# Optimization experiments

Measured on AMD Instinct MI355X. Metric: run time of the kernel, lower is better.

Reference implementation:

```python
import jax, jax.numpy as jnp
import numpy as np

B, T, D, H = 2, 2048, 1024, 16
HD = D // H


def setup_inputs() -> dict:
    key = jax.random.key(0)
    ks = jax.random.split(key, 8)
    s = 1.0 / np.sqrt(D)
    x = jax.random.normal(ks[0], (B, T, D), dtype=jnp.float32)
    # causal additive mask, as in Whisper: -inf-like on strict upper triangle
    mask = jnp.triu(jnp.full((T, T), -1e9, dtype=jnp.float32), k=1)
    Wq = jax.random.normal(ks[1], (D, D), dtype=jnp.float32) * s
    bq = jax.random.normal(ks[2], (D,), dtype=jnp.float32) * 0.02
    Wk = jax.random.normal(ks[3], (D, D), dtype=jnp.float32) * s  # key has no bias
    Wv = jax.random.normal(ks[4], (D, D), dtype=jnp.float32) * s
    bv = jax.random.normal(ks[5], (D,), dtype=jnp.float32) * 0.02
    Wo = jax.random.normal(ks[6], (D, D), dtype=jnp.float32) * s
    bo = jax.random.normal(ks[7], (D,), dtype=jnp.float32) * 0.02
    return {"x": x, "mask": mask, "Wq": Wq, "bq": bq, "Wk": Wk,
            "Wv": Wv, "bv": bv, "Wo": Wo, "bo": bo}


def reference(x, mask, Wq, bq, Wk, Wv, bv, Wo, bo):
    # Linear layers (torch F.linear: x @ W.T + b)
    q = x @ Wq.T + bq                      # [B, T, D]
    k = x @ Wk.T                           # [B, T, D] (no bias)
    v = x @ Wv.T + bv                      # [B, T, D]

    scale = (D // H) ** (-0.25)
    qh = q.reshape(B, T, H, HD) * scale    # [B, T, H, hd]
    kh = k.reshape(B, T, H, HD) * scale
    vh = v.reshape(B, T, H, HD)

    qk = jnp.einsum("bqhd,bkhd->bhqk", qh, kh)        # [B, H, T, T]
    qk = qk + mask[:T, :T]
    w = jax.nn.softmax(qk.astype(jnp.float32), axis=-1).astype(q.dtype)
    wv = jnp.einsum("bhqk,bkhd->bqhd", w, vh).reshape(B, T, D)
    return wv @ Wo.T + bo
```

## Files before the change

kernel.cpp:

```cpp
#include <hip/hip_runtime.h>
#include <hip/hip_bf16.h>

#define B_ 2
#define T_ 2048
#define D_ 1024
#define H_ 16
#define HD_ 64

typedef __attribute__((ext_vector_type(8))) short bf16x8;
typedef __attribute__((ext_vector_type(4))) short bf16x4;
typedef __attribute__((ext_vector_type(4))) float f32x4;
typedef __attribute__((ext_vector_type(4))) unsigned int u32x4;

__device__ __forceinline__ short f2bf(float f) {
  unsigned int u = __builtin_bit_cast(unsigned int, f);
  u += 0x7fffu + ((u >> 16) & 1u);
  return (short)(u >> 16);
}

__device__ __forceinline__ unsigned cvtpk(float lo, float hi) {
  unsigned r;
  asm("v_cvt_pk_bf16_f32 %0, %1, %2" : "=v"(r) : "v"(lo), "v"(hi));
  return r;
}

__device__ __forceinline__ float ex2(float x) {
  float r;
  asm("v_exp_f32 %0, %1" : "=v"(r) : "v"(x));
  return r;
}

__device__ __forceinline__ void gl16(const short* g, short* l) {
  __builtin_amdgcn_global_load_lds(
      (const __attribute__((address_space(1))) void*)g,
      (__attribute__((address_space(3))) void*)l, 16, 0, 0);
}

__global__ void cast_all(const float* __restrict__ x,
                         const float* __restrict__ w0, const float* __restrict__ w1,
                         const float* __restrict__ w2, const float* __restrict__ w3,
                         short* __restrict__ out) {
  int i = (blockIdx.x * blockDim.x + threadIdx.x) * 8;
  const float* src;
  int off;
  if (i < 4194304) { src = x; off = i; }
  else {
    int j = i - 4194304;
    int seg = j >> 20;
    src = (seg == 0) ? w0 : (seg == 1) ? w1 : (seg == 2) ? w2 : w3;
    off = j & 1048575;
  }
  float4 a = *(const float4*)(src + off);
  float4 b = *(const float4*)(src + off + 4);
  bf16x8 o;
  o[0] = f2bf(a.x); o[1] = f2bf(a.y); o[2] = f2bf(a.z); o[3] = f2bf(a.w);
  o[4] = f2bf(b.x); o[5] = f2bf(b.y); o[6] = f2bf(b.z); o[7] = f2bf(b.w);
  *(bf16x8*)(out + i) = o;
}

__launch_bounds__(256, 4)
__global__ void gemm_qkv(const short* __restrict__ A, const short* __restrict__ W,
                         const float* __restrict__ bq, const float* __restrict__ bv,
                         short* __restrict__ Qb, short* __restrict__ Kb,
                         short* __restrict__ Vtb) {
  __shared__ short As[2][128 * 32];
  __shared__ short Bs[2][128 * 32];
  const int xcd = blockIdx.x & 7, g = blockIdx.x >> 3;
  const int bm = (xcd >> 1) * 8 + (g & 7);
  const int bn = (xcd & 1) * 12 + (g >> 3);
  const int tid = threadIdx.x, lane = tid & 63, w = tid >> 6;
  const int wr = w >> 1, wc = w & 1;
  const int lrow = lane & 15, lhi = lane >> 4;
  const int srow = lane >> 2, sch = lane & 3;
  const int swz = (lrow >> 1) & 3;

  f32x4 acc[4][4] = {};
  auto STAGE = [&](int kt, int buf) {
#pragma unroll
    for (int i = 0; i < 2; ++i) {
      int row = w * 32 + i * 16 + srow;
      int csrc = (sch ^ ((row >> 1) & 3)) * 8;
      gl16(A + (size_t)(bm * 128 + row) * 1024 + kt + csrc,
           &As[buf][(w * 32 + i * 16) * 32]);
      gl16(W + (size_t)(bn * 128 + row) * 1024 + kt + csrc,
           &Bs[buf][(w * 32 + i * 16) * 32]);
    }
  };

  STAGE(0, 0);
  for (int t = 0; t < 32; ++t) {
    const int buf = t & 1;
    if (t < 31) {
      STAGE((t + 1) * 32, buf ^ 1);
      asm volatile("s_waitcnt vmcnt(4)" ::: "memory");
    } else {
      asm volatile("s_waitcnt vmcnt(0)" ::: "memory");
    }
    __builtin_amdgcn_s_barrier();
    bf16x8 af[4], bfr[4];
#pragma unroll
    for (int i = 0; i < 4; ++i) {
      af[i]  = *(const bf16x8*)(&As[buf][(wr * 64 + i * 16 + lrow) * 32 + ((lhi ^ swz) * 8)]);
      bfr[i] = *(const bf16x8*)(&Bs[buf][(wc * 64 + i * 16 + lrow) * 32 + ((lhi ^ swz) * 8)]);
    }
#pragma unroll
    for (int i = 0; i < 4; ++i)
#pragma unroll
      for (int j = 0; j < 4; ++j)
        acc[i][j] = __builtin_amdgcn_mfma_f32_16x16x32_bf16(af[i], bfr[j],
                                                            acc[i][j], 0, 0, 0);
    asm volatile("s_waitcnt lgkmcnt(0)" ::: "memory");
    __builtin_amdgcn_s_barrier();
  }

#pragma unroll
  for (int i = 0; i < 4; ++i)
#pragma unroll
    for (int j = 0; j < 4; ++j) {
      const int m0 = bm * 128 + wr * 64 + i * 16 + lhi * 4;
      const int n = bn * 128 + wc * 64 + j * 16 + lrow;
      const int seg = n >> 10, nloc = n & 1023;
      const int h = nloc >> 6, hd = nloc & 63;
      const int b = m0 >> 11, t0 = m0 & 2047;
      if (seg == 0) {
        float bb = bq[nloc];
#pragma unroll
        for (int r = 0; r < 4; ++r)
          Qb[((size_t)(b * H_ + h) * T_ + t0 + r) * HD_ + hd] =
              f2bf((acc[i][j][r] + bb) * 0.180336880f);
      } else if (seg == 1) {
#pragma unroll
        for (int r = 0; r < 4; ++r)
          Kb[((size_t)(b * H_ + h) * T_ + t0 + r) * HD_ + hd] = f2bf(acc[i][j][r]);
      } else {
        float bb = bv[nloc];
        bf16x4 ov;
#pragma unroll
        for (int r = 0; r < 4; ++r) ov[r] = f2bf(acc[i][j][r] + bb);
        const int c = (i >> 1) * 32 + lhi * 8 + (i & 1) * 4;
        *(bf16x4*)(Vtb + ((size_t)(b * H_ + h) * HD_ + hd) * T_ + (t0 & ~63) + c) = ov;
      }
    }
}

__launch_bounds__(256, 3)
__global__ void gemm_o(const short* __restrict__ A, const short* __restrict__ W,
                       const float* __restrict__ bias, float* __restrict__ out) {
  __shared__ short As[2][64 * 64];
  __shared__ short Bs[2][128 * 64];
  const int xcd = blockIdx.x & 7, g = blockIdx.x >> 3;
  const int bm = (xcd >> 1) * 16 + (g & 15);
  const int bn = (xcd & 1) * 4 + (g >> 4);
  const int tid = threadIdx.x, lane = tid & 63, w = tid >> 6;
  const int wr = w >> 1, wc = w & 1;
  const int lrow = lane & 15, lhi = lane >> 4;
  const int srow = lane >> 3, sch = lane & 7;
  const int swz = (lrow & 7) << 3;

  f32x4 acc[2][4] = {};
  auto STAGE = [&](int kt, int buf) {
#pragma unroll
    for (int i = 0; i < 2; ++i) {
      int row = w * 16 + i * 8 + srow;
      gl16(A + (size_t)(bm * 64 + row) * 1024 + kt + ((sch ^ (row & 7)) * 8),
           &As[buf][(w * 16 + i * 8) * 64]);
    }
#pragma unroll
    for (int i = 0; i < 4; ++i) {
      int row = w * 32 + i * 8 + srow;
      gl16(W + (size_t)(bn * 128 + row) * 1024 + kt + ((sch ^ (row & 7)) * 8),
           &Bs[buf][(w * 32 + i * 8) * 64]);
    }
  };

  STAGE(0, 0);
  for (int t = 0; t < 16; ++t) {
    const int buf = t & 1;
    if (t < 15) {
      STAGE((t + 1) * 64, buf ^ 1);
      asm volatile("s_waitcnt vmcnt(6)" ::: "memory");
    } else {
      asm volatile("s_waitcnt vmcnt(0)" ::: "memory");
    }
    __builtin_amdgcn_s_barrier();
    bf16x8 af[2][2], bfr[2][4];
#pragma unroll
    for (int ks = 0; ks < 2; ++ks) {
#pragma unroll
      for (int i = 0; i < 2; ++i)
        af[ks][i] = *(const bf16x8*)(&As[buf][(wr * 32 + i * 16 + lrow) * 64 + ((ks * 32 + lhi * 8) ^ swz)]);
#pragma unroll
      for (int j = 0; j < 4; ++j)
        bfr[ks][j] = *(const bf16x8*)(&Bs[buf][(wc * 64 + j * 16 + lrow) * 64 + ((ks * 32 + lhi * 8) ^ swz)]);
    }
#pragma unroll
    for (int ks = 0; ks < 2; ++ks)
#pragma unroll
      for (int i = 0; i < 2; ++i)
#pragma unroll
        for (int j = 0; j < 4; ++j)
          acc[i][j] = __builtin_amdgcn_mfma_f32_16x16x32_bf16(af[ks][i], bfr[ks][j],
                                                              acc[i][j], 0, 0, 0);
    asm volatile("s_waitcnt lgkmcnt(0)" ::: "memory");
    __builtin_amdgcn_s_barrier();
  }

#pragma unroll
  for (int i = 0; i < 2; ++i)
#pragma unroll
    for (int j = 0; j < 4; ++j) {
      const int m0 = bm * 64 + wr * 32 + i * 16 + lhi * 4;
      const int n = bn * 128 + wc * 64 + j * 16 + lrow;
      const float bb = bias[n];
#pragma unroll
      for (int r = 0; r < 4; ++r)
        out[(size_t)(m0 + r) * 1024 + n] = acc[i][j][r] + bb;
    }
}

__launch_bounds__(256, 4)
__global__ void attn_kernel(const short* __restrict__ Q, const short* __restrict__ K,
                            const short* __restrict__ Vt, short* __restrict__ Ob) {
  __shared__ short Ks_[2][64 * 64];
  __shared__ short Vs_[2][64 * 64];
  const int tid = threadIdx.x, lane = tid & 63, w = tid >> 6;
  const int lrow = lane & 15, lhi = lane >> 4;
  const int bid = blockIdx.x;
  const int bh = (bid & 7) * 4 + ((bid >> 3) & 3);
  const int x = bid >> 5, g = x & 7, q = x >> 3;
  const int tile = ((q & 1) ? (7 - g) : g) * 4 + q;
  const int b = bh >> 4, h = bh & 15;
  const short* Kbh = K + (size_t)bh * T_ * HD_;
  const short* Vbh = Vt + (size_t)bh * HD_ * T_;

  bf16x8 qf[2];
#pragma unroll
  for (int ks = 0; ks < 2; ++ks)
    qf[ks] = *(const bf16x8*)(Q + ((size_t)bh * T_ + tile * 64 + w * 16 + lrow) * HD_ + ks * 32 + lhi * 8);

  f32x4 oacc[4] = {};
  float lrun = 0.f;
  const int qlocal = w * 16 + lrow;
  const int srow8 = lane >> 3, sch = lane & 7;
  const int swz = (lrow & 7) << 3;

  auto STAGE = [&](int kb, int buf) {
#pragma unroll
    for (int pass = 0; pass < 2; ++pass) {
      int row = pass * 32 + w * 8 + srow8;
      int csrc = (sch ^ (row & 7)) * 8;
      gl16(Kbh + (size_t)(kb * 64 + row) * HD_ + csrc, &Ks_[buf][(pass * 32 + w * 8) * 64]);
      gl16(Vbh + (size_t)row * T_ + kb * 64 + csrc, &Vs_[buf][(pass * 32 + w * 8) * 64]);
    }
  };

  STAGE(0, 0);
  int cur = 0;
  for (int kb = 0; kb <= tile; ++kb) {
    asm volatile("s_waitcnt vmcnt(0) lgkmcnt(0)" ::: "memory");
    __builtin_amdgcn_s_barrier();
    asm volatile("" ::: "memory");
    const short* Kc = Ks_[cur];
    const short* Vc = Vs_[cur];
    bf16x8 kf[4][2];
#pragma unroll
    for (int n = 0; n < 4; ++n)
#pragma unroll
      for (int ks = 0; ks < 2; ++ks)
        kf[n][ks] = *(const bf16x8*)(Kc + (n * 16 + lrow) * 64 + ((ks * 32 + lhi * 8) ^ swz));
    bf16x8 vf[4][2];
#pragma unroll
    for (int j = 0; j < 4; ++j)
#pragma unroll
      for (int ks = 0; ks < 2; ++ks)
        vf[j][ks] = *(const bf16x8*)(Vc + (j * 16 + lrow) * 64 + ((ks * 32 + lhi * 8) ^ swz));
    if (kb < tile) STAGE(kb + 1, cur ^ 1);

    f32x4 s[4] = {};
    __builtin_amdgcn_s_setprio(1);
#pragma unroll
    for (int n = 0; n < 4; ++n)
#pragma unroll
      for (int ks = 0; ks < 2; ++ks)
        s[n] = __builtin_amdgcn_mfma_f32_16x16x32_bf16(kf[n][ks], qf[ks], s[n], 0, 0, 0);
    __builtin_amdgcn_s_setprio(0);

    if (kb == tile) {
#pragma unroll
      for (int n = 0; n < 4; ++n)
#pragma unroll
        for (int r = 0; r < 4; ++r)
          if (n * 16 + lhi * 4 + r > qlocal) s[n][r] = -1e9f;
    }

    float p[4][4];
    float ls = 0.f;
#pragma unroll
    for (int n = 0; n < 4; ++n)
#pragma unroll
      for (int r = 0; r < 4; ++r) {
        float e = ex2(s[n][r]);
        p[n][r] = e;
        ls += e;
      }
    lrun += ls;

    u32x4 pw0, pw1;
    pw0[0] = cvtpk(p[0][0], p[0][1]); pw0[1] = cvtpk(p[0][2], p[0][3]);
    pw0[2] = cvtpk(p[1][0], p[1][1]); pw0[3] = cvtpk(p[1][2], p[1][3]);
    pw1[0] = cvtpk(p[2][0], p[2][1]); pw1[1] = cvtpk(p[2][2], p[2][3]);
    pw1[2] = cvtpk(p[3][0], p[3][1]); pw1[3] = cvtpk(p[3][2], p[3][3]);
    bf16x8 pf0 = __builtin_bit_cast(bf16x8, pw0);
    bf16x8 pf1 = __builtin_bit_cast(bf16x8, pw1);

    __builtin_amdgcn_s_setprio(1);
#pragma unroll
    for (int j = 0; j < 4; ++j) {
      oacc[j] = __builtin_amdgcn_mfma_f32_16x16x32_bf16(vf[j][0], pf0, oacc[j], 0, 0, 0);
      oacc[j] = __builtin_amdgcn_mfma_f32_16x16x32_bf16(vf[j][1], pf1, oacc[j], 0, 0, 0);
    }
    __builtin_amdgcn_s_setprio(0);
    cur ^= 1;
  }

  lrun += __shfl_xor(lrun, 16);
  lrun += __shfl_xor(lrun, 32);
  float inv = 1.0f / lrun;
  const int t = tile * 64 + qlocal;
#pragma unroll
  for (int j = 0; j < 4; ++j) {
    bf16x4 ok;
#pragma unroll
    for (int r = 0; r < 4; ++r) ok[r] = f2bf(oacc[j][r] * inv);
    *(bf16x4*)(Ob + (size_t)(b * T_ + t) * D_ + h * 64 + j * 16 + lhi * 4) = ok;
  }
}

extern "C" void kernel_launch(void* const* d_in, const int* in_sizes, int n_in,
                              void* d_out, int out_size, void* d_ws, size_t ws_size,
                              hipStream_t stream) {
  const float* x  = (const float*)d_in[0];
  const float* Wq = (const float*)d_in[2];
  const float* bq = (const float*)d_in[3];
  const float* Wk = (const float*)d_in[4];
  const float* Wv = (const float*)d_in[5];
  const float* bv = (const float*)d_in[6];
  const float* Wo = (const float*)d_in[7];
  const float* bo = (const float*)d_in[8];
  float* out = (float*)d_out;

  const int MT = B_ * T_;
  short* xb  = (short*)d_ws;
  short* wqb = xb  + (size_t)MT * D_;
  short* wob = wqb + (size_t)3 * D_ * D_;
  short* Qb  = wob + (size_t)D_ * D_;
  short* Kb  = Qb  + (size_t)MT * D_;
  short* Vtb = Kb  + (size_t)MT * D_;
  short* Ab  = Vtb + (size_t)MT * D_;

  cast_all<<<(8 * 1048576) / (256 * 8), 256, 0, stream>>>(x, Wq, Wk, Wv, Wo, xb);

  gemm_qkv<<<(MT / 128) * 24, 256, 0, stream>>>(xb, wqb, bq, bv, Qb, Kb, Vtb);

  attn_kernel<<<B_ * H_ * 32, 256, 0, stream>>>(Qb, Kb, Vtb, Ab);

  gemm_o<<<(MT / 64) * 8, 256, 0, stream>>>(Ab, wob, bo, out);
}
```

Measured before the change: 90.84 us.

## Enlarge QKV GEMM tiles to 256x256 with 8 waves and 4-stage pipeline

The QKV projection GEMM now uses 256x256 output tiles computed by 512-thread blocks (8 waves, each 128x64), replacing 128x128 tiles with 4 waves. The LDS staging goes from double buffering to a 4-deep ring, issuing loads three k-steps ahead with matching vmcnt waits. It also raises wave priority around the MFMA block. The aim is more operand reuse per global load and better latency hiding. The cost is more registers and LDS per block and only 192 blocks for the GPU's CUs.

After: 105.1 us. +15.7%, slower.

```diff
diff --git a/kernel.cpp b/kernel.cpp
--- a/kernel.cpp
+++ b/kernel.cpp
@@ -58,67 +58,77 @@
   *(bf16x8*)(out + i) = o;
 }
 
-__launch_bounds__(256, 4)
+__launch_bounds__(512, 2)
 __global__ void gemm_qkv(const short* __restrict__ A, const short* __restrict__ W,
                          const float* __restrict__ bq, const float* __restrict__ bv,
                          short* __restrict__ Qb, short* __restrict__ Kb,
                          short* __restrict__ Vtb) {
-  __shared__ short As[2][128 * 32];
-  __shared__ short Bs[2][128 * 32];
-  const int xcd = blockIdx.x & 7, g = blockIdx.x >> 3;
-  const int bm = (xcd >> 1) * 8 + (g & 7);
-  const int bn = (xcd & 1) * 12 + (g >> 3);
-  const int tid = threadIdx.x, lane = tid & 63, w = tid >> 6;
-  const int wr = w >> 1, wc = w & 1;
+  __shared__ short As[4][256 * 32];
+  __shared__ short Bs[4][256 * 32];
+  const int xcd = blockIdx.x & 7, g24 = blockIdx.x >> 3;
+  const int bm = (xcd >> 1) * 4 + (g24 & 3);
+  const int bn = (xcd & 1) * 6 + (g24 >> 2);
+  const int tid = threadIdx.x, lane = tid & 63, wid = tid >> 6;
+  const int wr = wid >> 2, wc = wid & 3;
   const int lrow = lane & 15, lhi = lane >> 4;
-  const int srow = lane >> 2, sch = lane & 3;
+  const int srow4 = lane >> 2, sch4 = lane & 3;
   const int swz = (lrow >> 1) & 3;
 
-  f32x4 acc[4][4] = {};
+  f32x4 acc[8][4] = {};
+
   auto STAGE = [&](int kt, int buf) {
 #pragma unroll
     for (int i = 0; i < 2; ++i) {
-      int row = w * 32 + i * 16 + srow;
-      int csrc = (sch ^ ((row >> 1) & 3)) * 8;
-      gl16(A + (size_t)(bm * 128 + row) * 1024 + kt + csrc,
-           &As[buf][(w * 32 + i * 16) * 32]);
-      gl16(W + (size_t)(bn * 128 + row) * 1024 + kt + csrc,
-           &Bs[buf][(w * 32 + i * 16) * 32]);
+      int row = i * 128 + wid * 16 + srow4;
+      int csrc = (sch4 ^ ((row >> 1) & 3)) * 8;
+      gl16(A + (size_t)(bm * 256 + row) * 1024 + kt * 32 + csrc,
+           &As[buf][(i * 128 + wid * 16) * 32]);
+      gl16(W + (size_t)(bn * 256 + row) * 1024 + kt * 32 + csrc,
+           &Bs[buf][(i * 128 + wid * 16) * 32]);
     }
   };
 
   STAGE(0, 0);
+  STAGE(1, 1);
+  STAGE(2, 2);
   for (int t = 0; t < 32; ++t) {
-    const int buf = t & 1;
-    if (t < 31) {
-      STAGE((t + 1) * 32, buf ^ 1);
+    const int buf = t & 3;
+    if (t < 29) {
+      STAGE(t + 3, (t + 3) & 3);
+      asm volatile("s_waitcnt vmcnt(12)" ::: "memory");
+    } else if (t == 29) {
+      asm volatile("s_waitcnt vmcnt(8)" ::: "memory");
+    } else if (t == 30) {
       asm volatile("s_waitcnt vmcnt(4)" ::: "memory");
     } else {
       asm volatile("s_waitcnt vmcnt(0)" ::: "memory");
     }
     __builtin_amdgcn_s_barrier();
-    bf16x8 af[4], bfr[4];
-#pragma unroll
-    for (int i = 0; i < 4; ++i) {
-      af[i]  = *(const bf16x8*)(&As[buf][(wr * 64 + i * 16 + lrow) * 32 + ((lhi ^ swz) * 8)]);
-      bfr[i] = *(const bf16x8*)(&Bs[buf][(wc * 64 + i * 16 + lrow) * 32 + ((lhi ^ swz) * 8)]);
-    }
-#pragma unroll
-    for (int i = 0; i < 4; ++i)
+    bf16x8 af[8], bfr[4];
+#pragma unroll
+    for (int i = 0; i < 8; ++i)
+      af[i] = *(const bf16x8*)(&As[buf][(wr * 128 + i * 16 + lrow) * 32 + ((lhi ^ swz) * 8)]);
+#pragma unroll
+    for (int j = 0; j < 4; ++j)
+      bfr[j] = *(const bf16x8*)(&Bs[buf][(wc * 64 + j * 16 + lrow) * 32 + ((lhi ^ swz) * 8)]);
+    __builtin_amdgcn_s_setprio(1);
+#pragma unroll
+    for (int i = 0; i < 8; ++i)
 #pragma unroll
       for (int j = 0; j < 4; ++j)
         acc[i][j] = __builtin_amdgcn_mfma_f32_16x16x32_bf16(af[i], bfr[j],
                                                             acc[i][j], 0, 0, 0);
+    __builtin_amdgcn_s_setprio(0);
     asm volatile("s_waitcnt lgkmcnt(0)" ::: "memory");
     __builtin_amdgcn_s_barrier();
   }
 
 #pragma unroll
-  for (int i = 0; i < 4; ++i)
+  for (int i = 0; i < 8; ++i)
 #pragma unroll
     for (int j = 0; j < 4; ++j) {
-      const int m0 = bm * 128 + wr * 64 + i * 16 + lhi * 4;
-      const int n = bn * 128 + wc * 64 + j * 16 + lrow;
+      const int m0 = bm * 256 + wr * 128 + i * 16 + lhi * 4;
+      const int n = bn * 256 + wc * 64 + j * 16 + lrow;
       const int seg = n >> 10, nloc = n & 1023;
       const int h = nloc >> 6, hd = nloc & 63;
       const int b = m0 >> 11, t0 = m0 & 2047;
@@ -137,7 +147,7 @@
         bf16x4 ov;
 #pragma unroll
         for (int r = 0; r < 4; ++r) ov[r] = f2bf(acc[i][j][r] + bb);
-        const int c = (i >> 1) * 32 + lhi * 8 + (i & 1) * 4;
+        const int c = ((i >> 1) & 1) * 32 + lhi * 8 + (i & 1) * 4;
         *(bf16x4*)(Vtb + ((size_t)(b * H_ + h) * HD_ + hd) * T_ + (t0 & ~63) + c) = ov;
       }
     }
@@ -360,7 +370,7 @@
 
   cast_all<<<(8 * 1048576) / (256 * 8), 256, 0, stream>>>(x, Wq, Wk, Wv, Wo, xb);
 
-  gemm_qkv<<<(MT / 128) * 24, 256, 0, stream>>>(xb, wqb, bq, bv, Qb, Kb, Vtb);
+  gemm_qkv<<<(MT / 256) * 12, 512, 0, stream>>>(xb, wqb, bq, bv, Qb, Kb, Vtb);
 
   attn_kernel<<<B_ * H_ * 32, 256, 0, stream>>>(Qb, Kb, Vtb, Ab);
 
```
